# Performance work log

Hardware: AMD Instinct MI355X
Metric: run time of the kernel (lower is better)

The kernel has to match this reference:

```python
import jax, jax.numpy as jnp
import numpy as np

# Module config: point_dim=2, channels_in=16, channels_out=16, mlp_channels=[8,8], use_bias=False
# set_quad(24) -> N=24 Gauss-Legendre points per axis, decay_param=(24/4)**4
# set_output_locs(12) -> 12x12=144 output locations
N_QUAD = 24
M_SIDE = 12
CI = 16
CO = 16
HID = 8
PDIM = 2
BATCH = 32
DECAY = (N_QUAD / 4.0) ** 4  # 1296.0


def setup_inputs() -> dict:
    key = jax.random.key(0)
    ks = jax.random.split(key, 4)
    # Gauss-Legendre quadrature (glpair equivalent)
    qn, qw = np.polynomial.legendre.leggauss(N_QUAD)
    quad_nodes = jnp.asarray(qn, jnp.float32)
    quad_weights = jnp.asarray(qw, jnp.float32)
    # set_output_locs(M_SIDE): meshgrid('xy') of M_SIDE Gauss nodes, row k=i*m+j -> (n_j, n_i)
    on, _ = np.polynomial.legendre.leggauss(M_SIDE)
    on = jnp.asarray(on, jnp.float32)
    output_locs = jnp.stack([jnp.tile(on, M_SIDE), jnp.repeat(on, M_SIDE)], axis=-1)  # (144, 2)
    features = jax.random.normal(ks[0], (BATCH, CI, N_QUAD * N_QUAD), jnp.float32)
    # One Sin-MLP (2->8->8->1, no bias) per (out,in) channel pair; torch Linear init U(-1/sqrt(fan_in), +)
    def lin(k, fi, fo):
        b = 1.0 / np.sqrt(fi)
        return jax.random.uniform(k, (CO, CI, fi, fo), jnp.float32, -b, b)
    W1 = lin(ks[1], PDIM, HID)
    W2 = lin(ks[2], HID, HID)
    W3 = lin(ks[3], HID, 1)
    return dict(features=features, output_locs=output_locs, quad_nodes=quad_nodes,
                quad_weights=quad_weights, W1=W1, W2=W2, W3=W3)


def _forward(features, output_locs, quad_nodes, quad_weights, W1, W2, W3):
    n = quad_nodes.shape[0]
    # rquad(level=2) flattened: feature index k = i*n + j maps to node (n_j, n_i), weight w_i*w_j
    nodes2d = jnp.stack([jnp.tile(quad_nodes, n), jnp.repeat(quad_nodes, n)], axis=-1)  # (K, 2)
    w2d = jnp.repeat(quad_weights, n) * jnp.tile(quad_weights, n)                      # (K,)
    x = output_locs[:, None, :] - nodes2d[None, :, :]   # (M, K, 2) kernel eval offsets
    M, K, _ = x.shape
    xf = x.reshape(M * K, PDIM)                          # (P, 2), P = M*K
    # eval_MLPs: grouped tiny MLPs over all (out,in) pairs, Sin activations
    h = jnp.sin(jnp.einsum('pd,ocdh->ocph', xf, W1))     # (CO, CI, P, HID)
    h = jnp.sin(jnp.einsum('ocph,ochg->ocpg', h, W2))    # (CO, CI, P, HID)
    w = jnp.einsum('ocpg,ocg->ocp', h, W3[..., 0])       # (CO, CI, P)
    # bump: e * exp(-1/(1 - decay*||x||^4)) inside compact support, 0 outside
    da = DECAY * jnp.sum(xf * xf, axis=-1) ** 2          # decay * ||x||^4, (P,)
    inside = da < 1.0
    den = jnp.where(inside, 1.0 - da, 1.0)
    bump = jnp.where(inside, jnp.float32(np.e) * jnp.exp(-1.0 / den), 0.0)
    mesh_w = jnp.tile(w2d, M)                            # per p = m*K + k -> w2d[k]
    kern = (w * bump * mesh_w).reshape(CO, CI, M, K)
    # quadrature contraction over input channels and quadrature points
    return jnp.einsum('ocmk,bck->bom', kern, features)   # (B, CO, M)


def reference(features, output_locs, quad_nodes, quad_weights, W1, W2, W3):
    return _forward(features, output_locs, quad_nodes, quad_weights, W1, W2, W3)
```

## Files before the change

kernel.cpp:

```cpp
#include <hip/hip_runtime.h>
#include <math.h>


#define NQ 24
#define M_TOT 144
#define NB 32

__device__ __forceinline__ float sin_poly(float x) {
    float z = x * x;
    float r = fmaf(z, 2.7557313707070068e-06f, -1.9841269659586510e-04f);
    r = fmaf(z, r, 8.3333333332248946e-03f);
    r = fmaf(z, r, -1.6666666666666632e-01f);
    return fmaf(x * z, r, x);
}

__global__ __launch_bounds__(256)
void quadconv_kernel(const float* __restrict__ F,
                     const float* __restrict__ OL,
                     const float* __restrict__ QN,
                     const float* __restrict__ QW,
                     const float* __restrict__ W1,
                     const float* __restrict__ W2,
                     const float* __restrict__ W3,
                     float* __restrict__ OUT) {
    const int m = blockIdx.x;
    const int t = threadIdx.x;
    const int o = t >> 4;
    const int c = t & 15;

    __shared__ float qn_s[NQ], qw_s[NQ];
    __shared__ float f_s[512];

    if (t < NQ) { qn_s[t] = QN[t]; qw_s[t] = QW[t]; }

    float w1r[16], w2r[64], w3r[8];
    {
        const float4* p1 = (const float4*)(W1 + t * 16);
        #pragma unroll
        for (int i = 0; i < 4; ++i) ((float4*)w1r)[i] = p1[i];
        const float4* p2 = (const float4*)(W2 + t * 64);
        #pragma unroll
        for (int i = 0; i < 16; ++i) ((float4*)w2r)[i] = p2[i];
        const float4* p3 = (const float4*)(W3 + t * 8);
        #pragma unroll
        for (int i = 0; i < 2; ++i) ((float4*)w3r)[i] = p3[i];
    }

    const float ox = OL[2 * m];
    const float oy = OL[2 * m + 1];

    float acc[NB];
    #pragma unroll
    for (int b = 0; b < NB; ++b) acc[b] = 0.0f;

    __syncthreads();

    const float R2MAX = 1.0f / 36.0f;
    for (int ik = 0; ik < NQ; ++ik) {
        float x1 = oy - qn_s[ik];
        float x1sq = x1 * x1;
        if (x1sq >= R2MAX) continue;
        for (int jk = 0; jk < NQ; ++jk) {
            float x0 = ox - qn_s[jk];
            float r2 = fmaf(x0, x0, x1sq);
            float da = 1296.0f * r2 * r2;
            if (da >= 1.0f) continue;
            float bump = 2.718281828459045f * expf(-1.0f / (1.0f - da));
            float kscale = bump * qw_s[ik] * qw_s[jk];
            int k = ik * NQ + jk;

            __syncthreads();
            f_s[t]       = F[o * 9216 + c * 576 + k];
            f_s[t + 256] = F[(o + 16) * 9216 + c * 576 + k];
            __syncthreads();

            float h1[8];
            #pragma unroll
            for (int h = 0; h < 8; ++h)
                h1[h] = sin_poly(fmaf(x0, w1r[h], x1 * w1r[8 + h]));

            float wsum = 0.0f;
            #pragma unroll
            for (int g = 0; g < 8; ++g) {
                float z = h1[0] * w2r[g];
                #pragma unroll
                for (int h = 1; h < 8; ++h)
                    z = fmaf(h1[h], w2r[h * 8 + g], z);
                wsum = fmaf(sin_poly(z), w3r[g], wsum);
            }

            float kv = wsum * kscale;
            #pragma unroll
            for (int b = 0; b < NB; ++b)
                acc[b] = fmaf(kv, f_s[b * 16 + c], acc[b]);
        }
    }

    #pragma unroll
    for (int b = 0; b < NB; ++b) {
        float v = acc[b];
        v += __shfl_xor(v, 1);
        v += __shfl_xor(v, 2);
        v += __shfl_xor(v, 4);
        v += __shfl_xor(v, 8);
        acc[b] = v;
    }
    if (c == 0) {
        #pragma unroll
        for (int b = 0; b < NB; ++b)
            OUT[b * (16 * M_TOT) + o * M_TOT + m] = acc[b];
    }
}

extern "C" void kernel_launch(void* const* d_in, const int* in_sizes, int n_in,
                              void* d_out, int out_size, void* d_ws, size_t ws_size,
                              hipStream_t stream) {
    const float* F  = (const float*)d_in[0];
    const float* OL = (const float*)d_in[1];
    const float* QN = (const float*)d_in[2];
    const float* QW = (const float*)d_in[3];
    const float* W1 = (const float*)d_in[4];
    const float* W2 = (const float*)d_in[5];
    const float* W3 = (const float*)d_in[6];
    float* OUT = (float*)d_out;
    quadconv_kernel<<<dim3(M_TOT), dim3(256), 0, stream>>>(F, OL, QN, QW, W1, W2, W3, OUT);
}
```

Baseline: 103.9 us.

## Split quadrature rows across blocks with atomic accumulation and bulk feature staging

Parallelises over (quadrature row, output location) pairs instead of only output locations, so each block handles one ik row and exits early when that row lies outside the bump support. Each block stages all 24 feature columns of its row into shared memory in one vectorised load, which removes the per-point syncthreads pairs. Partial sums are combined with atomicAdd into an output zeroed by a memset, and launch bounds request two blocks per CU. The costs are an extra memset, atomic contention, a 48KB shared buffer that limits occupancy, and reloading the weights in every block.

```diff
diff --git a/kernel.cpp b/kernel.cpp
--- a/kernel.cpp
+++ b/kernel.cpp
@@ -14,7 +14,7 @@
     return fmaf(x * z, r, x);
 }
 
-__global__ __launch_bounds__(256)
+__global__ __launch_bounds__(256, 2)
 void quadconv_kernel(const float* __restrict__ F,
                      const float* __restrict__ OL,
                      const float* __restrict__ QN,
@@ -23,13 +23,22 @@
                      const float* __restrict__ W2,
                      const float* __restrict__ W3,
                      float* __restrict__ OUT) {
-    const int m = blockIdx.x;
-    const int t = threadIdx.x;
-    const int o = t >> 4;
-    const int c = t & 15;
+    const int ik = blockIdx.x;
+    const int m  = blockIdx.y;
+    const int t  = threadIdx.x;
+    const int o  = t >> 4;
+    const int c  = t & 15;
 
+    const float oy = OL[2 * m + 1];
+    const float x1 = oy - QN[ik];
+    const float x1sq = x1 * x1;
+    if (x1sq >= 1.0f / 36.0f) return;
+
+    const float ox   = OL[2 * m];
+    const float qwik = QW[ik];
+
+    __shared__ float f_s[NQ * 512];
     __shared__ float qn_s[NQ], qw_s[NQ];
-    __shared__ float f_s[512];
 
     if (t < NQ) { qn_s[t] = QN[t]; qw_s[t] = QW[t]; }
 
@@ -46,55 +55,62 @@
         for (int i = 0; i < 2; ++i) ((float4*)w3r)[i] = p3[i];
     }
 
-    const float ox = OL[2 * m];
-    const float oy = OL[2 * m + 1];
+    {
+        const int kbase = ik * NQ;
+        #pragma unroll
+        for (int pp = 0; pp < 2; ++pp) {
+            const int p  = t + pp * 256;
+            const int b  = p >> 4;
+            const int cc = p & 15;
+            const float4* src = (const float4*)(F + b * 9216 + cc * 576 + kbase);
+            float4 q[6];
+            #pragma unroll
+            for (int j = 0; j < 6; ++j) q[j] = src[j];
+            const float* qs = (const float*)q;
+            #pragma unroll
+            for (int j = 0; j < NQ; ++j) f_s[j * 512 + p] = qs[j];
+        }
+    }
+    __syncthreads();
 
     float acc[NB];
     #pragma unroll
     for (int b = 0; b < NB; ++b) acc[b] = 0.0f;
+    bool any = false;
 
-    __syncthreads();
+    for (int jk = 0; jk < NQ; ++jk) {
+        float x0 = ox - qn_s[jk];
+        float r2 = fmaf(x0, x0, x1sq);
+        float da = 1296.0f * r2 * r2;
+        if (da >= 1.0f) continue;
+        any = true;
 
-    const float R2MAX = 1.0f / 36.0f;
-    for (int ik = 0; ik < NQ; ++ik) {
-        float x1 = oy - qn_s[ik];
-        float x1sq = x1 * x1;
-        if (x1sq >= R2MAX) continue;
-        for (int jk = 0; jk < NQ; ++jk) {
-            float x0 = ox - qn_s[jk];
-            float r2 = fmaf(x0, x0, x1sq);
-            float da = 1296.0f * r2 * r2;
-            if (da >= 1.0f) continue;
-            float bump = 2.718281828459045f * expf(-1.0f / (1.0f - da));
-            float kscale = bump * qw_s[ik] * qw_s[jk];
-            int k = ik * NQ + jk;
+        float bump = 2.718281828459045f * expf(-1.0f / (1.0f - da));
+        float kscale = bump * qwik * qw_s[jk];
 
-            __syncthreads();
-            f_s[t]       = F[o * 9216 + c * 576 + k];
-            f_s[t + 256] = F[(o + 16) * 9216 + c * 576 + k];
-            __syncthreads();
+        float h1[8];
+        #pragma unroll
+        for (int h = 0; h < 8; ++h)
+            h1[h] = sin_poly(fmaf(x0, w1r[h], x1 * w1r[8 + h]));
 
-            float h1[8];
+        float wsum = 0.0f;
+        #pragma unroll
+        for (int g = 0; g < 8; ++g) {
+            float z = h1[0] * w2r[g];
             #pragma unroll
-            for (int h = 0; h < 8; ++h)
-                h1[h] = sin_poly(fmaf(x0, w1r[h], x1 * w1r[8 + h]));
+            for (int h = 1; h < 8; ++h)
+                z = fmaf(h1[h], w2r[h * 8 + g], z);
+            wsum = fmaf(sin_poly(z), w3r[g], wsum);
+        }
 
-            float wsum = 0.0f;
-            #pragma unroll
-            for (int g = 0; g < 8; ++g) {
-                float z = h1[0] * w2r[g];
-                #pragma unroll
-                for (int h = 1; h < 8; ++h)
-                    z = fmaf(h1[h], w2r[h * 8 + g], z);
-                wsum = fmaf(sin_poly(z), w3r[g], wsum);
-            }
+        float kv = wsum * kscale;
+        const float* fp = &f_s[jk * 512 + c];
+        #pragma unroll
+        for (int b = 0; b < NB; ++b)
+            acc[b] = fmaf(kv, fp[b * 16], acc[b]);
+    }
 
-            float kv = wsum * kscale;
-            #pragma unroll
-            for (int b = 0; b < NB; ++b)
-                acc[b] = fmaf(kv, f_s[b * 16 + c], acc[b]);
-        }
-    }
+    if (!any) return;
 
     #pragma unroll
     for (int b = 0; b < NB; ++b) {
@@ -108,7 +124,7 @@
     if (c == 0) {
         #pragma unroll
         for (int b = 0; b < NB; ++b)
-            OUT[b * (16 * M_TOT) + o * M_TOT + m] = acc[b];
+            atomicAdd(&OUT[b * (16 * M_TOT) + o * M_TOT + m], acc[b]);
     }
 }
 
@@ -123,5 +139,6 @@
     const float* W2 = (const float*)d_in[5];
     const float* W3 = (const float*)d_in[6];
     float* OUT = (float*)d_out;
-    quadconv_kernel<<<dim3(M_TOT), dim3(256), 0, stream>>>(F, OL, QN, QW, W1, W2, W3, OUT);
+    hipMemsetAsync(d_out, 0, (size_t)out_size * sizeof(float), stream);
+    quadconv_kernel<<<dim3(NQ, M_TOT), dim3(256), 0, stream>>>(F, OL, QN, QW, W1, W2, W3, OUT);
 }
```

Result: faster. 95.31 us (-8.2%).
